# Kernel tuning notes

Hardware: AMD Instinct MI355X
Metric: run time of the kernel (lower is better)

The kernel has to match this reference:

```python
import jax, jax.numpy as jnp
import numpy as np

B, S, D = 4, 2048, 1024


def setup_inputs() -> dict:
    key = jax.random.key(0)
    k1, k2, k3, k4 = jax.random.split(key, 4)
    x = jax.random.normal(k1, (B, S, D), dtype=jnp.float32)
    # 'random_normal' keras initializer uses stddev=0.05
    w_keys = jax.random.normal(k2, (D, D), dtype=jnp.float32) * 0.05
    w_queries = jax.random.normal(k3, (D, D), dtype=jnp.float32) * 0.05
    w_values = jax.random.normal(k4, (D, D), dtype=jnp.float32) * 0.05
    return {"x": x, "w_keys": w_keys, "w_queries": w_queries, "w_values": w_values}


def reference(x, w_keys, w_queries, w_values):
    # fact = sqrt(input feature dim)
    fact = jnp.sqrt(jnp.asarray(x.shape[-1], x.dtype))
    vk = x @ w_keys      # [B,S,D]
    vq = x @ w_queries   # [B,S,D]
    vv = x @ w_values    # [B,S,D]
    # NOTE: module computes K @ Q^T (keys as rows), softmax over last axis
    kq = jnp.einsum('bsd,btd->bst', vk, vq) / fact   # [B,S,S]
    sn = jax.nn.softmax(kq, axis=-1)
    # pm + transpose_b cancel: out = sn @ vv
    out = jnp.einsum('bst,btd->bsd', sn, vv)         # [B,S,D]
    return out
```

## Files before the change

### kernel.cpp

```cpp
#include <hip/hip_runtime.h>


typedef __attribute__((ext_vector_type(8))) short bf16x8;
typedef __attribute__((ext_vector_type(4))) float f32x4;

__device__ __forceinline__ unsigned short f2bf(float f) {
    unsigned int u = __float_as_uint(f);
    u += 0x7fff + ((u >> 16) & 1);
    return (unsigned short)(u >> 16);
}
__device__ __forceinline__ float bf2f(unsigned short s) {
    return __uint_as_float((unsigned int)s << 16);
}

__device__ __forceinline__ void gld_lds16(const unsigned short* g, unsigned short* l) {
    __builtin_amdgcn_global_load_lds(
        (const __attribute__((address_space(1))) void*)g,
        (__attribute__((address_space(3))) void*)l, 16, 0, 0);
}

template<int N> __device__ __forceinline__ void vmcnt_wait() {
    if constexpr (N == 0) asm volatile("s_waitcnt vmcnt(0)" ::: "memory");
    else if constexpr (N == 8) asm volatile("s_waitcnt vmcnt(8)" ::: "memory");
}
__device__ __forceinline__ void bar() {
    asm volatile("" ::: "memory");
    __builtin_amdgcn_s_barrier();
    asm volatile("" ::: "memory");
}

template<int KT, bool RS>
__device__ __forceinline__ void gemm4(
    const unsigned short* __restrict__ A, const unsigned short* __restrict__ B,
    int lda, int ldb, int bm, int bn,
    unsigned short* As, unsigned short* Bs,
    f32x4 (&acc)[4][4], float (&rs)[4])
{
    const int tid  = threadIdx.x;
    const int lane = tid & 63;
    const int wave = tid >> 6;
    const int wr = wave >> 1, wc = wave & 1;
    const int lr = lane & 15, kg = lane >> 4;

    const int srow = tid >> 2;
    const int ssrc = ((tid & 3) ^ ((tid >> 3) & 3)) * 8;
    const unsigned short* pa0 = A + (size_t)(bm + srow) * lda + ssrc;
    const unsigned short* pa1 = A + (size_t)(bm + 64 + srow) * lda + ssrc;
    const unsigned short* pb0 = B + (size_t)(bn + srow) * ldb + ssrc;
    const unsigned short* pb1 = B + (size_t)(bn + 64 + srow) * ldb + ssrc;

    const int phys = (kg ^ ((lr >> 1) & 3)) * 8;
    const int aoff = (wr * 64 + lr) * 32 + phys;
    const int boff = (wc * 64 + lr) * 32 + phys;

    auto stage = [&](int buf, int kt) {
        unsigned short* da = As + buf * 8192 + wave * 512;
        unsigned short* db = Bs + buf * 8192 + wave * 512;
        #pragma unroll
        for (int kh = 0; kh < 2; kh++) {
            const int go = kt * 64 + kh * 32;
            gld_lds16(pa0 + go, da + kh * 4096);
            gld_lds16(pa1 + go, da + kh * 4096 + 2048);
            gld_lds16(pb0 + go, db + kh * 4096);
            gld_lds16(pb1 + go, db + kh * 4096 + 2048);
        }
    };

    stage(0, 0);
    stage(1, 1);
    vmcnt_wait<8>();
    bar();

    for (int kt = 0; kt < KT; ++kt) {
        const int c = kt & 1;
        const unsigned short* Ab = As + c * 8192 + aoff;
        const unsigned short* Bb = Bs + c * 8192 + boff;

        #pragma unroll
        for (int kh = 0; kh < 2; kh++) {
            bf16x8 af[4], bf[4];
            #pragma unroll
            for (int mf = 0; mf < 4; mf++)
                af[mf] = *reinterpret_cast<const bf16x8*>(Ab + kh * 4096 + mf * 512);
            #pragma unroll
            for (int nf = 0; nf < 4; nf++)
                bf[nf] = *reinterpret_cast<const bf16x8*>(Bb + kh * 4096 + nf * 512);
            __builtin_amdgcn_s_setprio(1);
            #pragma unroll
            for (int mf = 0; mf < 4; mf++)
                #pragma unroll
                for (int nf = 0; nf < 4; nf++)
                    acc[mf][nf] = __builtin_amdgcn_mfma_f32_16x16x32_bf16(af[mf], bf[nf], acc[mf][nf], 0, 0, 0);
            __builtin_amdgcn_s_setprio(0);
            if constexpr (RS) {
                #pragma unroll
                for (int mf = 0; mf < 4; mf++)
                    #pragma unroll
                    for (int e = 0; e < 8; e++) rs[mf] += bf2f(((unsigned short*)&af[mf])[e]);
            }
        }

        if (kt == KT - 1) break;
        bar();
        if (kt + 2 < KT) {
            stage(c, kt + 2);
            vmcnt_wait<8>();
        } else {
            vmcnt_wait<0>();
        }
        bar();
    }
}

__global__ __launch_bounds__(256) void convert_bf16(
    const float* __restrict__ src, unsigned short* __restrict__ dst)
{
    const size_t idx = (size_t)blockIdx.x * 256 + threadIdx.x;
    const float4* xi = reinterpret_cast<const float4*>(src) + idx * 2;
    float4 v0 = xi[0], v1 = xi[1];
    ushort4 a = { f2bf(v0.x), f2bf(v0.y), f2bf(v0.z), f2bf(v0.w) };
    ushort4 b = { f2bf(v1.x), f2bf(v1.y), f2bf(v1.z), f2bf(v1.w) };
    ushort4* xo = reinterpret_cast<ushort4*>(dst) + idx * 2;
    xo[0] = a; xo[1] = b;
}

__global__ __launch_bounds__(256) void transpose_w1(
    const float* __restrict__ w, unsigned short* __restrict__ o)
{
    __shared__ unsigned short T[64][72];
    const int k0 = blockIdx.y * 64, n0 = blockIdx.x * 64;
    const int tid = threadIdx.x;
    const int r = tid >> 4, c4 = (tid & 15) * 4;
    #pragma unroll
    for (int i = 0; i < 4; i++) {
        int kr = r + i * 16;
        float4 v = *reinterpret_cast<const float4*>(&w[(size_t)(k0 + kr) * 1024 + n0 + c4]);
        T[c4 + 0][kr] = f2bf(v.x);
        T[c4 + 1][kr] = f2bf(v.y);
        T[c4 + 2][kr] = f2bf(v.z);
        T[c4 + 3][kr] = f2bf(v.w);
    }
    __syncthreads();
    #pragma unroll
    for (int i = 0; i < 4; i++) {
        int n = r + i * 16;
        ushort4 v = *reinterpret_cast<const ushort4*>(&T[n][c4]);
        *reinterpret_cast<ushort4*>(&o[(size_t)(n0 + n) * 1024 + k0 + c4]) = v;
    }
}

__global__ __launch_bounds__(256, 2) void g_gemm(
    const unsigned short* __restrict__ wqb, const unsigned short* __restrict__ wkb,
    unsigned short* __restrict__ Gt)
{
    __shared__ unsigned short As[2 * 128 * 64], Bs[2 * 128 * 64];
    const int bid = blockIdx.x;
    const int wg  = (bid & 7) * 8 + (bid >> 3);
    const int bm  = (wg >> 3) * 128;
    const int bn  = (wg & 7) * 128;

    f32x4 acc[4][4] = {};
    float rs[4] = {};
    gemm4<16, false>(wqb, wkb, 1024, 1024, bm, bn, As, Bs, acc, rs);

    const int tid = threadIdx.x, lane = tid & 63, wave = tid >> 6;
    const int wr = wave >> 1, wc = wave & 1, lr = lane & 15, kg = lane >> 4;
    #pragma unroll
    for (int mf = 0; mf < 4; mf++)
        #pragma unroll
        for (int nf = 0; nf < 4; nf++)
            #pragma unroll
            for (int r = 0; r < 4; r++)
                Gt[(size_t)(bm + wr * 64 + mf * 16 + kg * 4 + r) * 1024
                   + bn + wc * 64 + nf * 16 + lr] = f2bf(acc[mf][nf][r]);
}

__global__ __launch_bounds__(256, 2) void proj_gemm(
    const unsigned short* __restrict__ xb, const unsigned short* __restrict__ Gt,
    const unsigned short* __restrict__ wvT,
    unsigned short* __restrict__ y, unsigned short* __restrict__ vvT)
{
    __shared__ unsigned short As[2 * 128 * 64], Bs[2 * 128 * 64];
    const int bid = blockIdx.x;
    const int wg  = (bid & 7) * 128 + (bid >> 3);
    const int z   = wg >> 9;
    const int rem = wg & 511;
    const int bm  = (rem >> 3) * 128;
    const int bn  = (rem & 7) * 128;
    const unsigned short* Bw = z ? wvT : Gt;

    f32x4 acc[4][4] = {};
    float rs[4] = {};
    gemm4<16, false>(xb, Bw, 1024, 1024, bm, bn, As, Bs, acc, rs);

    const int tid = threadIdx.x, lane = tid & 63, wave = tid >> 6;
    const int wr = wave >> 1, wc = wave & 1, lr = lane & 15, kg = lane >> 4;
    if (z == 0) {
        #pragma unroll
        for (int mf = 0; mf < 4; mf++)
            #pragma unroll
            for (int nf = 0; nf < 4; nf++)
                #pragma unroll
                for (int r = 0; r < 4; r++)
                    y[(size_t)(bm + wr * 64 + mf * 16 + kg * 4 + r) * 1024
                      + bn + wc * 64 + nf * 16 + lr] = f2bf(acc[mf][nf][r]);
    } else {
        const int batch = bm >> 11;
        unsigned short* o = vvT + (size_t)batch * 1024 * 2048;
        #pragma unroll
        for (int mf = 0; mf < 4; mf++)
            #pragma unroll
            for (int nf = 0; nf < 4; nf++) {
                ushort4 v = { f2bf(acc[mf][nf][0]), f2bf(acc[mf][nf][1]),
                              f2bf(acc[mf][nf][2]), f2bf(acc[mf][nf][3]) };
                *reinterpret_cast<ushort4*>(
                    &o[(size_t)(bn + wc * 64 + nf * 16 + lr) * 2048
                       + (bm & 2047) + wr * 64 + mf * 16 + kg * 4]) = v;
            }
    }
}

__global__ __launch_bounds__(256, 2) void scores_gemm(
    const unsigned short* __restrict__ y, const unsigned short* __restrict__ xb,
    unsigned short* __restrict__ P)
{
    __shared__ unsigned short As[2 * 128 * 64], Bs[2 * 128 * 64];
    const int bid = blockIdx.x;
    const int wg  = (bid & 7) * 128 + (bid >> 3);
    const int z   = wg >> 8;
    const int rem = wg & 255;
    const int bm  = (rem >> 4) * 128;
    const int bn  = (rem & 15) * 128;
    const unsigned short* A = y  + (size_t)z * 2048 * 1024;
    const unsigned short* B = xb + (size_t)z * 2048 * 1024;
    unsigned short* out = P + (size_t)z * 2048 * 2048;

    f32x4 acc[4][4] = {};
    float rs[4] = {};
    gemm4<16, false>(A, B, 1024, 1024, bm, bn, As, Bs, acc, rs);

    const int tid = threadIdx.x, lane = tid & 63, wave = tid >> 6;
    const int wr = wave >> 1, wc = wave & 1, lr = lane & 15, kg = lane >> 4;
    #pragma unroll
    for (int mf = 0; mf < 4; mf++)
        #pragma unroll
        for (int nf = 0; nf < 4; nf++)
            #pragma unroll
            for (int r = 0; r < 4; r++)
                out[(size_t)(bm + wr * 64 + mf * 16 + kg * 4 + r) * 2048
                    + bn + wc * 64 + nf * 16 + lr]
                    = f2bf(__expf(acc[mf][nf][r] * 0.03125f));
}

__global__ __launch_bounds__(256, 2) void pv_gemm(
    const unsigned short* __restrict__ P, const unsigned short* __restrict__ vvT,
    float* __restrict__ out)
{
    __shared__ unsigned short As[2 * 128 * 64], Bs[2 * 128 * 64];
    const int bid = blockIdx.x;
    const int wg  = (bid & 7) * 64 + (bid >> 3);
    const int z   = wg >> 7;
    const int rem = wg & 127;
    const int bm  = (rem >> 3) * 128;
    const int bn  = (rem & 7) * 128;
    const unsigned short* A = P   + (size_t)z * 2048 * 2048;
    const unsigned short* B = vvT + (size_t)z * 1024 * 2048;
    float* o = out + (size_t)z * 2048 * 1024;

    f32x4 acc[4][4] = {};
    float rs[4] = {};
    gemm4<32, true>(A, B, 2048, 2048, bm, bn, As, Bs, acc, rs);

    const int tid = threadIdx.x, lane = tid & 63, wave = tid >> 6;
    const int wr = wave >> 1, wc = wave & 1, lr = lane & 15, kg = lane >> 4;

    #pragma unroll
    for (int mf = 0; mf < 4; mf++) {
        rs[mf] += __shfl_xor(rs[mf], 16);
        rs[mf] += __shfl_xor(rs[mf], 32);
    }
    #pragma unroll
    for (int mf = 0; mf < 4; mf++)
        #pragma unroll
        for (int r = 0; r < 4; r++) {
            const float l = __shfl(rs[mf], kg * 4 + r);
            const float inv = 1.0f / l;
            #pragma unroll
            for (int nf = 0; nf < 4; nf++)
                o[(size_t)(bm + wr * 64 + mf * 16 + kg * 4 + r) * 1024
                  + bn + wc * 64 + nf * 16 + lr] = acc[mf][nf][r] * inv;
        }
}

extern "C" void kernel_launch(void* const* d_in, const int* in_sizes, int n_in,
                              void* d_out, int out_size, void* d_ws, size_t ws_size,
                              hipStream_t stream) {
    const float* x  = (const float*)d_in[0];
    const float* wk = (const float*)d_in[1];
    const float* wq = (const float*)d_in[2];
    const float* wv = (const float*)d_in[3];
    float* out = (float*)d_out;

    char* ws = (char*)d_ws;
    const size_t MB = 1024 * 1024;
    unsigned short* xb  = (unsigned short*)(ws);
    unsigned short* y   = (unsigned short*)(ws + 16 * MB);
    unsigned short* wqb = (unsigned short*)(ws + 32 * MB);
    unsigned short* wkb = (unsigned short*)(ws + 34 * MB);
    unsigned short* Gt  = (unsigned short*)(ws + 36 * MB);
    unsigned short* wvT = (unsigned short*)(ws + 38 * MB);
    unsigned short* vvT = (unsigned short*)(ws + 40 * MB);
    unsigned short* P   = (unsigned short*)(ws + 56 * MB);

    convert_bf16<<<dim3(4096),     256, 0, stream>>>(x,  xb);
    convert_bf16<<<dim3(512),      256, 0, stream>>>(wq, wqb);
    convert_bf16<<<dim3(512),      256, 0, stream>>>(wk, wkb);
    transpose_w1<<<dim3(16, 16),   256, 0, stream>>>(wv, wvT);
    g_gemm      <<<dim3(64),       256, 0, stream>>>(wqb, wkb, Gt);
    proj_gemm   <<<dim3(1024),     256, 0, stream>>>(xb, Gt, wvT, y, vvT);
    scores_gemm <<<dim3(1024),     256, 0, stream>>>(y, xb, P);
    pv_gemm     <<<dim3(512),      256, 0, stream>>>(P, vvT, out);
}
```

Baseline: 172.0 us.

## Fuse preprocessing kernels into one launch and compute row sums via MFMA

Merges the x conversion, the Wv transpose, and the Wq·Wk^T product into a single stage1 kernel. The G GEMM now converts fp32 weights on the fly in 64x64 tiles, with no double buffering. This cuts the pipeline from eight launches to four and drops the wqb/wkb intermediate buffers. In pv_gemm the per-row softmax denominator is now computed with an extra MFMA against a vector of ones instead of scalar bf16 adds and lane shuffles. The price is a slower, unpipelined small GEMM and a few extra MFMA instructions inside the PV loop.

```diff
diff --git a/kernel.cpp b/kernel.cpp
--- a/kernel.cpp
+++ b/kernel.cpp
@@ -8,9 +8,6 @@
     unsigned int u = __float_as_uint(f);
     u += 0x7fff + ((u >> 16) & 1);
     return (unsigned short)(u >> 16);
-}
-__device__ __forceinline__ float bf2f(unsigned short s) {
-    return __uint_as_float((unsigned int)s << 16);
 }
 
 __device__ __forceinline__ void gld_lds16(const unsigned short* g, unsigned short* l) {
@@ -34,13 +31,16 @@
     const unsigned short* __restrict__ A, const unsigned short* __restrict__ B,
     int lda, int ldb, int bm, int bn,
     unsigned short* As, unsigned short* Bs,
-    f32x4 (&acc)[4][4], float (&rs)[4])
+    f32x4 (&acc)[4][4], f32x4 (&os)[4])
 {
     const int tid  = threadIdx.x;
     const int lane = tid & 63;
     const int wave = tid >> 6;
     const int wr = wave >> 1, wc = wave & 1;
     const int lr = lane & 15, kg = lane >> 4;
+
+    const bf16x8 ONES = { (short)0x3F80, (short)0x3F80, (short)0x3F80, (short)0x3F80,
+                          (short)0x3F80, (short)0x3F80, (short)0x3F80, (short)0x3F80 };
 
     const int srow = tid >> 2;
     const int ssrc = ((tid & 3) ^ ((tid >> 3) & 3)) * 8;
@@ -91,13 +91,12 @@
                 #pragma unroll
                 for (int nf = 0; nf < 4; nf++)
                     acc[mf][nf] = __builtin_amdgcn_mfma_f32_16x16x32_bf16(af[mf], bf[nf], acc[mf][nf], 0, 0, 0);
-            __builtin_amdgcn_s_setprio(0);
             if constexpr (RS) {
                 #pragma unroll
                 for (int mf = 0; mf < 4; mf++)
-                    #pragma unroll
-                    for (int e = 0; e < 8; e++) rs[mf] += bf2f(((unsigned short*)&af[mf])[e]);
+                    os[mf] = __builtin_amdgcn_mfma_f32_16x16x32_bf16(af[mf], ONES, os[mf], 0, 0, 0);
             }
+            __builtin_amdgcn_s_setprio(0);
         }
 
         if (kt == KT - 1) break;
@@ -112,67 +111,109 @@
     }
 }
 
-__global__ __launch_bounds__(256) void convert_bf16(
-    const float* __restrict__ src, unsigned short* __restrict__ dst)
-{
-    const size_t idx = (size_t)blockIdx.x * 256 + threadIdx.x;
-    const float4* xi = reinterpret_cast<const float4*>(src) + idx * 2;
-    float4 v0 = xi[0], v1 = xi[1];
-    ushort4 a = { f2bf(v0.x), f2bf(v0.y), f2bf(v0.z), f2bf(v0.w) };
-    ushort4 b = { f2bf(v1.x), f2bf(v1.y), f2bf(v1.z), f2bf(v1.w) };
-    ushort4* xo = reinterpret_cast<ushort4*>(dst) + idx * 2;
-    xo[0] = a; xo[1] = b;
-}
-
-__global__ __launch_bounds__(256) void transpose_w1(
-    const float* __restrict__ w, unsigned short* __restrict__ o)
-{
-    __shared__ unsigned short T[64][72];
-    const int k0 = blockIdx.y * 64, n0 = blockIdx.x * 64;
+__global__ __launch_bounds__(256) void stage1(
+    const float* __restrict__ x,  unsigned short* __restrict__ xb,
+    const float* __restrict__ wv, unsigned short* __restrict__ wvT,
+    const float* __restrict__ wq, const float* __restrict__ wk,
+    unsigned short* __restrict__ Gt)
+{
+    __shared__ unsigned short SM[4608];
+    const int bid = blockIdx.x;
     const int tid = threadIdx.x;
-    const int r = tid >> 4, c4 = (tid & 15) * 4;
+
+    if (bid < 4096) {
+        const size_t idx = (size_t)bid * 256 + tid;
+        const float4* xi = reinterpret_cast<const float4*>(x) + idx * 2;
+        float4 v0 = xi[0], v1 = xi[1];
+        ushort4 a = { f2bf(v0.x), f2bf(v0.y), f2bf(v0.z), f2bf(v0.w) };
+        ushort4 b = { f2bf(v1.x), f2bf(v1.y), f2bf(v1.z), f2bf(v1.w) };
+        ushort4* xo = reinterpret_cast<ushort4*>(xb) + idx * 2;
+        xo[0] = a; xo[1] = b;
+        return;
+    }
+    if (bid < 4352) {
+        auto T = reinterpret_cast<unsigned short (*)[72]>(SM);
+        const int tb = bid - 4096;
+        const int k0 = (tb >> 4) * 64, n0 = (tb & 15) * 64;
+        const int r = tid >> 4, c4 = (tid & 15) * 4;
+        #pragma unroll
+        for (int i = 0; i < 4; i++) {
+            int kr = r + i * 16;
+            float4 v = *reinterpret_cast<const float4*>(&wv[(size_t)(k0 + kr) * 1024 + n0 + c4]);
+            T[c4 + 0][kr] = f2bf(v.x);
+            T[c4 + 1][kr] = f2bf(v.y);
+            T[c4 + 2][kr] = f2bf(v.z);
+            T[c4 + 3][kr] = f2bf(v.w);
+        }
+        __syncthreads();
+        #pragma unroll
+        for (int i = 0; i < 4; i++) {
+            int n = r + i * 16;
+            ushort4 v = *reinterpret_cast<const ushort4*>(&T[n][c4]);
+            *reinterpret_cast<ushort4*>(&wvT[(size_t)(n0 + n) * 1024 + k0 + c4]) = v;
+        }
+        return;
+    }
+
+    unsigned short* As = SM;
+    unsigned short* Bs = SM + 2048;
+    const int gb = bid - 4352;
+    const int bm = (gb >> 4) * 64, bn = (gb & 15) * 64;
+
+    const int lane = tid & 63;
+    const int wave = tid >> 6;
+    const int wr = wave >> 1, wc = wave & 1;
+    const int lr = lane & 15, kg = lane >> 4;
+
+    const int srow = tid >> 2;
+    const int su   = tid & 3;
+    const int sphys = (su ^ ((srow >> 1) & 3)) * 8;
+    const int rphys = (kg ^ ((lr >> 1) & 3)) * 8;
+    const int aoff = (wr * 32 + lr) * 32 + rphys;
+    const int boff = (wc * 32 + lr) * 32 + rphys;
+
+    f32x4 acc[2][2] = {};
+
+    for (int k0 = 0; k0 < 1024; k0 += 32) {
+        {
+            const float* pa = &wq[(size_t)(bm + srow) * 1024 + k0 + su * 8];
+            float4 v0 = *reinterpret_cast<const float4*>(pa);
+            float4 v1 = *reinterpret_cast<const float4*>(pa + 4);
+            ushort4 u0 = { f2bf(v0.x), f2bf(v0.y), f2bf(v0.z), f2bf(v0.w) };
+            ushort4 u1 = { f2bf(v1.x), f2bf(v1.y), f2bf(v1.z), f2bf(v1.w) };
+            *reinterpret_cast<ushort4*>(&As[srow * 32 + sphys])     = u0;
+            *reinterpret_cast<ushort4*>(&As[srow * 32 + sphys + 4]) = u1;
+            const float* pb = &wk[(size_t)(bn + srow) * 1024 + k0 + su * 8];
+            float4 w0 = *reinterpret_cast<const float4*>(pb);
+            float4 w1 = *reinterpret_cast<const float4*>(pb + 4);
+            ushort4 t0 = { f2bf(w0.x), f2bf(w0.y), f2bf(w0.z), f2bf(w0.w) };
+            ushort4 t1 = { f2bf(w1.x), f2bf(w1.y), f2bf(w1.z), f2bf(w1.w) };
+            *reinterpret_cast<ushort4*>(&Bs[srow * 32 + sphys])     = t0;
+            *reinterpret_cast<ushort4*>(&Bs[srow * 32 + sphys + 4]) = t1;
+        }
+        __syncthreads();
+        bf16x8 af[2], bf[2];
+        #pragma unroll
+        for (int mf = 0; mf < 2; mf++)
+            af[mf] = *reinterpret_cast<const bf16x8*>(&As[aoff + mf * 512]);
+        #pragma unroll
+        for (int nf = 0; nf < 2; nf++)
+            bf[nf] = *reinterpret_cast<const bf16x8*>(&Bs[boff + nf * 512]);
+        #pragma unroll
+        for (int mf = 0; mf < 2; mf++)
+            #pragma unroll
+            for (int nf = 0; nf < 2; nf++)
+                acc[mf][nf] = __builtin_amdgcn_mfma_f32_16x16x32_bf16(af[mf], bf[nf], acc[mf][nf], 0, 0, 0);
+        __syncthreads();
+    }
     #pragma unroll
-    for (int i = 0; i < 4; i++) {
-        int kr = r + i * 16;
-        float4 v = *reinterpret_cast<const float4*>(&w[(size_t)(k0 + kr) * 1024 + n0 + c4]);
-        T[c4 + 0][kr] = f2bf(v.x);
-        T[c4 + 1][kr] = f2bf(v.y);
-        T[c4 + 2][kr] = f2bf(v.z);
-        T[c4 + 3][kr] = f2bf(v.w);
-    }
-    __syncthreads();
-    #pragma unroll
-    for (int i = 0; i < 4; i++) {
-        int n = r + i * 16;
-        ushort4 v = *reinterpret_cast<const ushort4*>(&T[n][c4]);
-        *reinterpret_cast<ushort4*>(&o[(size_t)(n0 + n) * 1024 + k0 + c4]) = v;
-    }
-}
-
-__global__ __launch_bounds__(256, 2) void g_gemm(
-    const unsigned short* __restrict__ wqb, const unsigned short* __restrict__ wkb,
-    unsigned short* __restrict__ Gt)
-{
-    __shared__ unsigned short As[2 * 128 * 64], Bs[2 * 128 * 64];
-    const int bid = blockIdx.x;
-    const int wg  = (bid & 7) * 8 + (bid >> 3);
-    const int bm  = (wg >> 3) * 128;
-    const int bn  = (wg & 7) * 128;
-
-    f32x4 acc[4][4] = {};
-    float rs[4] = {};
-    gemm4<16, false>(wqb, wkb, 1024, 1024, bm, bn, As, Bs, acc, rs);
-
-    const int tid = threadIdx.x, lane = tid & 63, wave = tid >> 6;
-    const int wr = wave >> 1, wc = wave & 1, lr = lane & 15, kg = lane >> 4;
-    #pragma unroll
-    for (int mf = 0; mf < 4; mf++)
-        #pragma unroll
-        for (int nf = 0; nf < 4; nf++)
+    for (int mf = 0; mf < 2; mf++)
+        #pragma unroll
+        for (int nf = 0; nf < 2; nf++)
             #pragma unroll
             for (int r = 0; r < 4; r++)
-                Gt[(size_t)(bm + wr * 64 + mf * 16 + kg * 4 + r) * 1024
-                   + bn + wc * 64 + nf * 16 + lr] = f2bf(acc[mf][nf][r]);
+                Gt[(size_t)(bm + wr * 32 + mf * 16 + kg * 4 + r) * 1024
+                   + bn + wc * 32 + nf * 16 + lr] = f2bf(acc[mf][nf][r]);
 }
 
 __global__ __launch_bounds__(256, 2) void proj_gemm(
@@ -190,8 +231,8 @@
     const unsigned short* Bw = z ? wvT : Gt;
 
     f32x4 acc[4][4] = {};
-    float rs[4] = {};
-    gemm4<16, false>(xb, Bw, 1024, 1024, bm, bn, As, Bs, acc, rs);
+    f32x4 os[4] = {};
+    gemm4<16, false>(xb, Bw, 1024, 1024, bm, bn, As, Bs, acc, os);
 
     const int tid = threadIdx.x, lane = tid & 63, wave = tid >> 6;
     const int wr = wave >> 1, wc = wave & 1, lr = lane & 15, kg = lane >> 4;
@@ -236,8 +277,8 @@
     unsigned short* out = P + (size_t)z * 2048 * 2048;
 
     f32x4 acc[4][4] = {};
-    float rs[4] = {};
-    gemm4<16, false>(A, B, 1024, 1024, bm, bn, As, Bs, acc, rs);
+    f32x4 os[4] = {};
+    gemm4<16, false>(A, B, 1024, 1024, bm, bn, As, Bs, acc, os);
 
     const int tid = threadIdx.x, lane = tid & 63, wave = tid >> 6;
     const int wr = wave >> 1, wc = wave & 1, lr = lane & 15, kg = lane >> 4;
@@ -268,23 +309,17 @@
     float* o = out + (size_t)z * 2048 * 1024;
 
     f32x4 acc[4][4] = {};
-    float rs[4] = {};
-    gemm4<32, true>(A, B, 2048, 2048, bm, bn, As, Bs, acc, rs);
+    f32x4 os[4] = {};
+    gemm4<32, true>(A, B, 2048, 2048, bm, bn, As, Bs, acc, os);
 
     const int tid = threadIdx.x, lane = tid & 63, wave = tid >> 6;
     const int wr = wave >> 1, wc = wave & 1, lr = lane & 15, kg = lane >> 4;
 
     #pragma unroll
-    for (int mf = 0; mf < 4; mf++) {
-        rs[mf] += __shfl_xor(rs[mf], 16);
-        rs[mf] += __shfl_xor(rs[mf], 32);
-    }
-    #pragma unroll
     for (int mf = 0; mf < 4; mf++)
         #pragma unroll
         for (int r = 0; r < 4; r++) {
-            const float l = __shfl(rs[mf], kg * 4 + r);
-            const float inv = 1.0f / l;
+            const float inv = 1.0f / os[mf][r];
             #pragma unroll
             for (int nf = 0; nf < 4; nf++)
                 o[(size_t)(bm + wr * 64 + mf * 16 + kg * 4 + r) * 1024
@@ -305,19 +340,13 @@
     const size_t MB = 1024 * 1024;
     unsigned short* xb  = (unsigned short*)(ws);
     unsigned short* y   = (unsigned short*)(ws + 16 * MB);
-    unsigned short* wqb = (unsigned short*)(ws + 32 * MB);
-    unsigned short* wkb = (unsigned short*)(ws + 34 * MB);
-    unsigned short* Gt  = (unsigned short*)(ws + 36 * MB);
-    unsigned short* wvT = (unsigned short*)(ws + 38 * MB);
-    unsigned short* vvT = (unsigned short*)(ws + 40 * MB);
-    unsigned short* P   = (unsigned short*)(ws + 56 * MB);
-
-    convert_bf16<<<dim3(4096),     256, 0, stream>>>(x,  xb);
-    convert_bf16<<<dim3(512),      256, 0, stream>>>(wq, wqb);
-    convert_bf16<<<dim3(512),      256, 0, stream>>>(wk, wkb);
-    transpose_w1<<<dim3(16, 16),   256, 0, stream>>>(wv, wvT);
-    g_gemm      <<<dim3(64),       256, 0, stream>>>(wqb, wkb, Gt);
-    proj_gemm   <<<dim3(1024),     256, 0, stream>>>(xb, Gt, wvT, y, vvT);
-    scores_gemm <<<dim3(1024),     256, 0, stream>>>(y, xb, P);
-    pv_gemm     <<<dim3(512),      256, 0, stream>>>(P, vvT, out);
-}
+    unsigned short* Gt  = (unsigned short*)(ws + 32 * MB);
+    unsigned short* wvT = (unsigned short*)(ws + 34 * MB);
+    unsigned short* vvT = (unsigned short*)(ws + 36 * MB);
+    unsigned short* P   = (unsigned short*)(ws + 52 * MB);
+
+    stage1     <<<dim3(4608), 256, 0, stream>>>(x, xb, wv, wvT, wq, wk, Gt);
+    proj_gemm  <<<dim3(1024), 256, 0, stream>>>(xb, Gt, wvT, y, vvT);
+    scores_gemm<<<dim3(1024), 256, 0, stream>>>(y, xb, P);
+    pv_gemm    <<<dim3(512),  256, 0, stream>>>(P, vvT, out);
+}
```

Measured after the change: 169.3 us. No clear change (-1.6%).
